# Kernel tuning notes

Measured on AMD Instinct MI355X. Metric: run time of the kernel, lower is better.

## Reference

```python
import jax, jax.numpy as jnp
import numpy as np

EPS = 1e-5  # BatchNorm2d default eps


def _binarize_ste(x):
    """Forward: sign(x). Backward: hardtanh STE (grad 1 where |x|<=1, else 0)."""
    xc = jnp.clip(x, -1.0, 1.0)
    return xc + jax.lax.stop_gradient(jnp.sign(x) - xc)


def setup_inputs() -> dict:
    key = jax.random.key(0)
    k1, k2, k3, k4 = jax.random.split(key, 4)
    x = jax.random.normal(k1, (32, 256, 32, 32), dtype=jnp.float32)
    # BatchNorm affine params (affine=True)
    gamma = 1.0 + 0.1 * jax.random.normal(k2, (256,), dtype=jnp.float32)
    beta = 0.1 * jax.random.normal(k3, (256,), dtype=jnp.float32)
    # Conv weight, OIHW, bias=False
    W = 0.05 * jax.random.normal(k4, (256, 256, 3, 3), dtype=jnp.float32)
    return {"x": x, "gamma": gamma, "beta": beta, "W": W}


def reference(x, gamma, beta, W):
    # BatchNorm2d, training-mode batch statistics over (N, H, W) per channel
    mean = jnp.mean(x, axis=(0, 2, 3), keepdims=True)
    var = jnp.var(x, axis=(0, 2, 3), keepdims=True)
    xn = (x - mean) * jax.lax.rsqrt(var + EPS)
    xn = xn * gamma[None, :, None, None] + beta[None, :, None, None]
    # Conv2d_1w1a: binarize activations and weights (sign fwd / STE bwd), then conv
    a = _binarize_ste(xn)
    wb = _binarize_ste(W)
    out = jax.lax.conv_general_dilated(
        a, wb,
        window_strides=(1, 1),
        padding=((1, 1), (1, 1)),
        dimension_numbers=("NCHW", "OIHW", "NCHW"),
    )
    return out
```

## Files before the change

kernel.cpp:

```cpp
#include <hip/hip_runtime.h>
#include <hip/hip_bf16.h>


#define NIMG 32
#define C    256
#define K    256

typedef int v4i  __attribute__((ext_vector_type(4)));
typedef int v16i __attribute__((ext_vector_type(16)));

#define AHT_IMG 295936
#define AHT_KB  36992
#define AHT_ROW 1088

__global__ __launch_bounds__(256) void k_stats_part(
    const float* __restrict__ x, double2* __restrict__ partials) {
  int grp = blockIdx.x;
  int c = blockIdx.y;
  int tid = threadIdx.x;
  double s = 0.0, sq = 0.0;
  #pragma unroll
  for (int ni = 0; ni < 4; ++ni) {
    int n = grp * 4 + ni;
    const float* p = x + (size_t)n * (C * 1024) + (size_t)c * 1024;
    float4 v = ((const float4*)p)[tid];
    s += (double)v.x + (double)v.y + (double)v.z + (double)v.w;
    sq += (double)v.x * v.x + (double)v.y * v.y
        + (double)v.z * v.z + (double)v.w * v.w;
  }
  for (int o = 32; o > 0; o >>= 1) {
    s += __shfl_down(s, o);
    sq += __shfl_down(sq, o);
  }
  __shared__ double ls[4], lq[4];
  if ((tid & 63) == 0) { ls[tid >> 6] = s; lq[tid >> 6] = sq; }
  __syncthreads();
  if (tid == 0) {
    double2 r;
    r.x = ls[0] + ls[1] + ls[2] + ls[3];
    r.y = lq[0] + lq[1] + lq[2] + lq[3];
    partials[c * 8 + grp] = r;
  }
}


__global__ __launch_bounds__(256) void k_packw_i8_final(
    const float* __restrict__ W, const double2* __restrict__ partials,
    const float* __restrict__ gamma, const float* __restrict__ beta,
    char* __restrict__ wfrag, float* __restrict__ t_out,
    unsigned* __restrict__ flip_out) {
  int bk = blockIdx.x;
  int tid = threadIdx.x;
  if (bk == 256) {
    int c = tid;
    double S = 0.0, Q = 0.0;
    #pragma unroll
    for (int g = 0; g < 8; ++g) {
      double2 p = partials[c * 8 + g];
      S += p.x; Q += p.y;
    }
    const double N = 32768.0;
    double mean = S / N;
    double var = Q / N - mean * mean;
    double rs = 1.0 / sqrt(var + 1e-5);
    double g = (double)gamma[c];
    double b = (double)beta[c];
    float t;
    unsigned flip;
    if (g == 0.0) {
      t = (b > 0.0) ? -3.0e38f : 3.0e38f;
      flip = 0u;
    } else {
      t = (float)(mean - b / (rs * g));
      flip = (g < 0.0) ? 1u : 0u;
    }
    t_out[c] = t;
    flip_out[c] = flip;
    return;
  }
  int k = bk, c = tid;
  const float* src = W + ((size_t)k * 256 + c) * 9;
  char* dst = wfrag + (size_t)(c >> 4) * 4096 + k * 16 + (c & 15);
  #pragma unroll
  for (int t = 0; t < 9; ++t)
    dst[(size_t)t * 65536] = (src[t] > 0.0f) ? (char)1 : (char)-1;
}

__global__ __launch_bounds__(256) void k_packa_i8(
    const float* __restrict__ x, const float* __restrict__ thr,
    const unsigned* __restrict__ flip, char* __restrict__ aHT) {
  __shared__ float lf[32 * 257];
  __shared__ float lthr[256];
  __shared__ unsigned lfl[256];
  int y = blockIdx.x, n = blockIdx.y, tid = threadIdx.x;
  lthr[tid] = thr[tid];
  lfl[tid] = flip[tid];
  #pragma unroll
  for (int it = 0; it < 8; ++it) {
    int c = it * 32 + (tid >> 3), q = tid & 7;
    float4 v = *(const float4*)(x + (size_t)n * 262144 + (size_t)c * 1024
                                + y * 32 + q * 4);
    lf[(q * 4 + 0) * 257 + c] = v.x;
    lf[(q * 4 + 1) * 257 + c] = v.y;
    lf[(q * 4 + 2) * 257 + c] = v.z;
    lf[(q * 4 + 3) * 257 + c] = v.w;
  }
  __syncthreads();
  int xl = tid & 31, cb = tid >> 5;
  unsigned wds[8];
  #pragma unroll
  for (int g = 0; g < 8; ++g) {
    unsigned wv = 0;
    #pragma unroll
    for (int jj = 0; jj < 4; ++jj) {
      int c = cb * 32 + g * 4 + jj;
      float v = lf[xl * 257 + c];
      unsigned bit = ((v > lthr[c]) ? 1u : 0u) ^ lfl[c];
      unsigned byte = bit ? 0x01u : 0xFFu;
      wv |= byte << (8 * jj);
    }
    wds[g] = wv;
  }
  char* dst = aHT + ((size_t)n * 8 + cb) * AHT_KB
            + (size_t)(y + 1) * AHT_ROW + (size_t)(xl + 1) * 32;
  uint4 u0, u1;
  u0.x = wds[0]; u0.y = wds[1]; u0.z = wds[2]; u0.w = wds[3];
  u1.x = wds[4]; u1.y = wds[5]; u1.z = wds[6]; u1.w = wds[7];
  *(uint4*)dst = u0;
  *((uint4*)dst + 1) = u1;

  uint4 z; z.x = 0; z.y = 0; z.z = 0; z.w = 0;
  if (xl < 2) {
    char* hz = aHT + ((size_t)n * 8 + cb) * AHT_KB
             + (size_t)(y + 1) * AHT_ROW + (size_t)(xl * 33) * 32;
    *(uint4*)hz = z;
    *((uint4*)hz + 1) = z;
  }
  if (y == 0 || y == 31) {
    int row = (y == 0) ? 0 : 33;
    for (int idx = tid; idx < 272; idx += 256) {
      int kb = idx / 34, xx = idx % 34;
      char* hz = aHT + ((size_t)n * 8 + kb) * AHT_KB
               + (size_t)row * AHT_ROW + (size_t)xx * 32;
      *(uint4*)hz = z;
      *((uint4*)hz + 1) = z;
    }
  }
}

__global__ __launch_bounds__(256) void k_conv_mfma(
    const char* __restrict__ aHT, const char* __restrict__ wfrag,
    float* __restrict__ out) {
  __shared__ uint4 lb4[2048];
  char* lb = (char*)lb4;
  int tid = threadIdx.x;
  int lane = tid & 63, nh = tid >> 6;
  int bx = blockIdx.x;
  int n = bx >> 4, ys = bx & 15;
  int y0 = ys * 2;
  int xl = lane & 31, hi = lane >> 5;

  const char* abT = aHT + (size_t)n * AHT_IMG + (size_t)(xl + 1) * 32 + hi * 16;
  const char* wsrc0 = wfrag + tid * 16;
  unsigned ldso = (unsigned)(tid * 16);
  unsigned bofs = (unsigned)(hi * 4096 + (nh * 64 + xl) * 16);

  v16i a00 = {0}, a01 = {0}, a10 = {0}, a11 = {0};
  v4i cA00, cA01, cA10, cA11;
  v4i nA00, nA01, nA10, nA11;
  uint4 wt0, wt1, wt2, wt3;

  cA00 = *(const v4i*)(abT + (size_t)(y0 + 0) * AHT_ROW - 32);
  cA01 = *(const v4i*)(abT + (size_t)(y0 + 1) * AHT_ROW - 32);
  cA10 = *(const v4i*)(abT + AHT_KB + (size_t)(y0 + 0) * AHT_ROW - 32);
  cA11 = *(const v4i*)(abT + AHT_KB + (size_t)(y0 + 1) * AHT_ROW - 32);
  wt0 = *(const uint4*)(wsrc0 + 0 * 4096);
  wt1 = *(const uint4*)(wsrc0 + 1 * 4096);
  wt2 = *(const uint4*)(wsrc0 + 2 * 4096);
  wt3 = *(const uint4*)(wsrc0 + 3 * 4096);
  *(uint4*)(lb + 0 * 4096 + ldso) = wt0;
  *(uint4*)(lb + 1 * 4096 + ldso) = wt1;
  *(uint4*)(lb + 2 * 4096 + ldso) = wt2;
  *(uint4*)(lb + 3 * 4096 + ldso) = wt3;
  __syncthreads();

  for (int p = 0; p < 36; ++p) {
    int buf = (p & 1) << 14;
    int nbuf = 16384 - buf;
    if (p < 35) {
      int kk0 = 2 * (p + 1);
      int tt = kk0 >> 3, kb0 = kk0 & 7;
      int dy = tt / 3 - 1, dx = (tt % 3) - 1;
      const char* ab = abT + (size_t)kb0 * AHT_KB
                     + (size_t)(y0 + dy + 1) * AHT_ROW + dx * 32;
      nA00 = *(const v4i*)(ab);
      nA01 = *(const v4i*)(ab + AHT_ROW);
      nA10 = *(const v4i*)(ab + AHT_KB);
      nA11 = *(const v4i*)(ab + AHT_KB + AHT_ROW);
      const char* wsrc = wsrc0 + (size_t)kk0 * 8192;
      wt0 = *(const uint4*)(wsrc + 0 * 4096);
      wt1 = *(const uint4*)(wsrc + 1 * 4096);
      wt2 = *(const uint4*)(wsrc + 2 * 4096);
      wt3 = *(const uint4*)(wsrc + 3 * 4096);
    }
    {
      const char* bp0 = lb + buf + bofs;
      v4i b0 = *(const v4i*)(bp0);
      v4i b1 = *(const v4i*)(bp0 + 512);
      a00 = __builtin_amdgcn_mfma_i32_32x32x32_i8(cA00, b0, a00, 0, 0, 0);
      a01 = __builtin_amdgcn_mfma_i32_32x32x32_i8(cA00, b1, a01, 0, 0, 0);
      a10 = __builtin_amdgcn_mfma_i32_32x32x32_i8(cA01, b0, a10, 0, 0, 0);
      a11 = __builtin_amdgcn_mfma_i32_32x32x32_i8(cA01, b1, a11, 0, 0, 0);
      const char* bp1 = lb + buf + 8192 + bofs;
      v4i b2 = *(const v4i*)(bp1);
      v4i b3 = *(const v4i*)(bp1 + 512);
      a00 = __builtin_amdgcn_mfma_i32_32x32x32_i8(cA10, b2, a00, 0, 0, 0);
      a01 = __builtin_amdgcn_mfma_i32_32x32x32_i8(cA10, b3, a01, 0, 0, 0);
      a10 = __builtin_amdgcn_mfma_i32_32x32x32_i8(cA11, b2, a10, 0, 0, 0);
      a11 = __builtin_amdgcn_mfma_i32_32x32x32_i8(cA11, b3, a11, 0, 0, 0);
    }
    if (p < 35) {
      cA00 = nA00; cA01 = nA01; cA10 = nA10; cA11 = nA11;
      *(uint4*)(lb + nbuf + 0 * 4096 + ldso) = wt0;
      *(uint4*)(lb + nbuf + 1 * 4096 + ldso) = wt1;
      *(uint4*)(lb + nbuf + 2 * 4096 + ldso) = wt2;
      *(uint4*)(lb + nbuf + 3 * 4096 + ldso) = wt3;
      __syncthreads();
    }
  }

  size_t ob0 = (size_t)n * 262144 + (size_t)(nh * 64 + xl) * 1024
             + (size_t)y0 * 32 + 4 * hi;
  #pragma unroll
  for (int r = 0; r < 2; ++r) {
    #pragma unroll
    for (int nb = 0; nb < 2; ++nb) {
      v16i av = (r == 0) ? (nb == 0 ? a00 : a01) : (nb == 0 ? a10 : a11);
      float* obp = out + ob0 + (size_t)nb * 32768 + r * 32;
      #pragma unroll
      for (int q = 0; q < 4; ++q) {
        float4 f;
        f.x = (float)av[q * 4 + 0];
        f.y = (float)av[q * 4 + 1];
        f.z = (float)av[q * 4 + 2];
        f.w = (float)av[q * 4 + 3];
        *(float4*)(obp + 8 * q) = f;
      }
    }
  }
}


__global__ __launch_bounds__(256) void k_packw_corr_final(
    const float* __restrict__ W, const double2* __restrict__ partials,
    const float* __restrict__ gamma, const float* __restrict__ beta,
    unsigned* __restrict__ wp, int* __restrict__ corr,
    unsigned* __restrict__ zp, float* __restrict__ t_out,
    unsigned* __restrict__ flip_out) {
  int bk = blockIdx.x;
  int tid = threadIdx.x;
  if (bk == 256) {
    int c = tid;
    double S = 0.0, Q = 0.0;
    #pragma unroll
    for (int g = 0; g < 8; ++g) {
      double2 p = partials[c * 8 + g];
      S += p.x; Q += p.y;
    }
    const double N = 32768.0;
    double mean = S / N;
    double var = Q / N - mean * mean;
    double rs = 1.0 / sqrt(var + 1e-5);
    double g = (double)gamma[c];
    double b = (double)beta[c];
    float t;
    unsigned flip;
    if (g == 0.0) {
      t = (b > 0.0) ? -3.0e38f : 3.0e38f;
      flip = 0u;
    } else {
      t = (float)(mean - b / (rs * g));
      flip = (g < 0.0) ? 1u : 0u;
    }
    t_out[c] = t;
    flip_out[c] = flip;
    return;
  }
  int k = bk;
  __shared__ unsigned lw[72];
  float w[9];
  const float* src = W + (size_t)k * 2304 + (size_t)tid * 9;
  #pragma unroll
  for (int t = 0; t < 9; ++t) w[t] = src[t];
  int lane = tid & 63, wv = tid >> 6;
  #pragma unroll
  for (int t = 0; t < 9; ++t) {
    unsigned long long m = __ballot(w[t] > 0.0f);
    if (lane == 0) {
      lw[t * 8 + 2 * wv] = (unsigned)m;
      lw[t * 8 + 2 * wv + 1] = (unsigned)(m >> 32);
    }
  }
  __syncthreads();
  if (tid < 72) wp[(size_t)k * 72 + tid] = lw[tid];
  if (tid >= 128 && tid < 144) {
    int cls = tid - 128;
    int sum = 0;
    #pragma unroll
    for (int t = 0; t < 9; ++t) {
      int dy = t / 3 - 1, dx = t % 3 - 1;
      bool inv = (((cls & 1) && dx == -1) || ((cls & 2) && dx == 1) ||
                  ((cls & 4) && dy == -1) || ((cls & 8) && dy == 1));
      if (inv) {
        #pragma unroll
        for (int j = 0; j < 8; ++j) sum += __popc(lw[t * 8 + j]);
      }
    }
    corr[k * 16 + cls] = sum;
  }
  if (bk == 0 && tid >= 192 && tid < 200) zp[tid - 192] = 0u;
}

__global__ __launch_bounds__(256) void k_packa_bits(
    const float* __restrict__ x, const float* __restrict__ t,
    const unsigned* __restrict__ flip, unsigned* __restrict__ ap) {
  int n = blockIdx.y;
  int p0 = blockIdx.x * 64;
  int pix = threadIdx.x & 63;
  int q = threadIdx.x >> 6;
  unsigned w0 = 0, w1 = 0;
  const float* xb = x + (size_t)n * (C * 1024) + p0 + pix;
  #pragma unroll
  for (int i = 0; i < 64; ++i) {
    int c = q * 64 + i;
    float tv = t[c];
    unsigned fl = flip[c];
    float v = xb[(size_t)c * 1024];
    unsigned bit = ((v > tv) ? 1u : 0u) ^ fl;
    if (i < 32) w0 |= bit << i;
    else        w1 |= bit << (i - 32);
  }
  uint2 st; st.x = w0; st.y = w1;
  *(uint2*)(ap + ((size_t)n * 1024 + p0 + pix) * 8 + q * 2) = st;
}

__global__ __launch_bounds__(256) void k_conv_pop(
    const unsigned* __restrict__ ap, const unsigned* __restrict__ wp,
    const int* __restrict__ corr, const unsigned* __restrict__ zp,
    float* __restrict__ out) {
  int n = blockIdx.z;
  int ystrip = blockIdx.y;
  int kc = blockIdx.x;
  int tid = threadIdx.x;
  int lane = tid & 63;
  int wave = tid >> 6;
  int y = ystrip * 8 + wave * 2 + (lane >> 5);
  int xx = lane & 31;
  int cls = (xx == 0 ? 1 : 0) | (xx == 31 ? 2 : 0) |
            (y == 0 ? 4 : 0) | (y == 31 ? 8 : 0);
  uint4 a0[9], a1[9];
  int nv = 0;
  const uint4* zp4 = (const uint4*)zp;
  #pragma unroll
  for (int t = 0; t < 9; ++t) {
    int dy = t / 3 - 1, dx = t % 3 - 1;
    int cy = y + dy, cx = xx + dx;
    bool valid = (cy >= 0) & (cy < 32) & (cx >= 0) & (cx < 32);
    nv += valid ? 1 : 0;
    const uint4* pa = valid
        ? (const uint4*)(ap + (((size_t)n * 32 + cy) * 32 + cx) * 8)
        : zp4;
    a0[t] = pa[0];
    a1[t] = pa[1];
  }
  int bias = nv << 8;
  float* ob = out + (size_t)n * (K * 1024) + (size_t)y * 32 + xx;
  for (int kk = 0; kk < 16; ++kk) {
    int k = kc * 16 + kk;
    const uint4* wq = (const uint4*)(wp + (size_t)k * 72);
    int s0 = 0, s1 = 0, s2 = 0, s3 = 0, s4 = 0, s5 = 0, s6 = 0, s7 = 0;
    #pragma unroll
    for (int t = 0; t < 9; ++t) {
      uint4 wa = wq[t * 2];
      uint4 wb = wq[t * 2 + 1];
      s0 += __popc(a0[t].x ^ wa.x);
      s1 += __popc(a0[t].y ^ wa.y);
      s2 += __popc(a0[t].z ^ wa.z);
      s3 += __popc(a0[t].w ^ wa.w);
      s4 += __popc(a1[t].x ^ wb.x);
      s5 += __popc(a1[t].y ^ wb.y);
      s6 += __popc(a1[t].z ^ wb.z);
      s7 += __popc(a1[t].w ^ wb.w);
    }
    int S = ((s0 + s1) + (s2 + s3)) + ((s4 + s5) + (s6 + s7));
    int tot = corr[(k << 4) + cls] - S;
    ob[(size_t)k * 1024] = (float)(bias + 2 * tot);
  }
}


extern "C" void kernel_launch(void* const* d_in, const int* in_sizes, int n_in,
                              void* d_out, int out_size, void* d_ws, size_t ws_size,
                              hipStream_t stream) {
  const float* x = (const float*)d_in[0];
  const float* gamma = (const float*)d_in[1];
  const float* beta = (const float*)d_in[2];
  const float* W = (const float*)d_in[3];
  float* out = (float*)d_out;
  char* ws = (char*)d_ws;

  const size_t NEED = 655360 + (size_t)NIMG * AHT_IMG;
  if (ws_size >= NEED) {
    float* t = (float*)ws;
    unsigned* flip = (unsigned*)(ws + 1024);
    double2* partials = (double2*)(ws + 4096);
    char* wfrag = ws + 36864;
    char* aHT = ws + 655360;

    k_stats_part<<<dim3(8, 256), 256, 0, stream>>>(x, partials);
    k_packw_i8_final<<<257, 256, 0, stream>>>(W, partials, gamma, beta,
                                              wfrag, t, flip);
    k_packa_i8<<<dim3(32, 32), 256, 0, stream>>>(x, t, flip, aHT);
    k_conv_mfma<<<512, 256, 0, stream>>>(aHT, wfrag, out);
  } else {
    float* t = (float*)ws;
    unsigned* flip = (unsigned*)(ws + 1024);
    unsigned* wp = (unsigned*)(ws + 4096);
    unsigned* zp = (unsigned*)(ws + 77824);
    int* corr = (int*)(ws + 78336);
    double2* partials = (double2*)(ws + 98304);
    unsigned* ap = (unsigned*)(ws + 131072);

    k_stats_part<<<dim3(8, 256), 256, 0, stream>>>(x, partials);
    k_packw_corr_final<<<257, 256, 0, stream>>>(W, partials, gamma, beta,
                                                wp, corr, zp, t, flip);
    k_packa_bits<<<dim3(16, 32), 256, 0, stream>>>(x, t, flip, ap);
    k_conv_pop<<<dim3(16, 4, 32), 256, 0, stream>>>(ap, wp, corr, zp, out);
  }
}
```

Baseline: 54.33 us.

## Share LDS weight tiles across two row-pairs with 512-thread conv blocks

The MFMA conv kernel now runs 512-thread blocks, 256 of them, and each block covers four output rows instead of two. Two groups of four waves share each LDS weight stage, so every thread loads half as many weight vectors per stage and total weight traffic from global memory is halved. The cost is fewer, larger blocks (256 for 256 CUs), a larger barrier scope and possibly lower occupancy.

```diff
diff --git a/kernel.cpp b/kernel.cpp
--- a/kernel.cpp
+++ b/kernel.cpp
@@ -148,60 +148,58 @@
   }
 }
 
-__global__ __launch_bounds__(256) void k_conv_mfma(
+__global__ __launch_bounds__(512) void k_conv_mfma(
     const char* __restrict__ aHT, const char* __restrict__ wfrag,
     float* __restrict__ out) {
   __shared__ uint4 lb4[2048];
   char* lb = (char*)lb4;
   int tid = threadIdx.x;
-  int lane = tid & 63, nh = tid >> 6;
+  int lane = tid & 63, w = tid >> 6;
   int bx = blockIdx.x;
-  int n = bx >> 4, ys = bx & 15;
-  int y0 = ys * 2;
+  int n = bx >> 3, ys = bx & 7;
+  int mb = w >> 2, nh = w & 3;
+  int yw = ys * 4 + mb * 2;
   int xl = lane & 31, hi = lane >> 5;
 
   const char* abT = aHT + (size_t)n * AHT_IMG + (size_t)(xl + 1) * 32 + hi * 16;
-  const char* wsrc0 = wfrag + tid * 16;
-  unsigned ldso = (unsigned)(tid * 16);
+  const char* wsrcA = wfrag + tid * 16;
+  unsigned ldsoA = (unsigned)(tid * 16);
   unsigned bofs = (unsigned)(hi * 4096 + (nh * 64 + xl) * 16);
 
   v16i a00 = {0}, a01 = {0}, a10 = {0}, a11 = {0};
   v4i cA00, cA01, cA10, cA11;
   v4i nA00, nA01, nA10, nA11;
-  uint4 wt0, wt1, wt2, wt3;
-
-  cA00 = *(const v4i*)(abT + (size_t)(y0 + 0) * AHT_ROW - 32);
-  cA01 = *(const v4i*)(abT + (size_t)(y0 + 1) * AHT_ROW - 32);
-  cA10 = *(const v4i*)(abT + AHT_KB + (size_t)(y0 + 0) * AHT_ROW - 32);
-  cA11 = *(const v4i*)(abT + AHT_KB + (size_t)(y0 + 1) * AHT_ROW - 32);
-  wt0 = *(const uint4*)(wsrc0 + 0 * 4096);
-  wt1 = *(const uint4*)(wsrc0 + 1 * 4096);
-  wt2 = *(const uint4*)(wsrc0 + 2 * 4096);
-  wt3 = *(const uint4*)(wsrc0 + 3 * 4096);
-  *(uint4*)(lb + 0 * 4096 + ldso) = wt0;
-  *(uint4*)(lb + 1 * 4096 + ldso) = wt1;
-  *(uint4*)(lb + 2 * 4096 + ldso) = wt2;
-  *(uint4*)(lb + 3 * 4096 + ldso) = wt3;
+  uint4 wt0, wt1;
+
+  {
+    const char* ab = abT + (size_t)yw * AHT_ROW - 32;
+    cA00 = *(const v4i*)(ab);
+    cA01 = *(const v4i*)(ab + AHT_ROW);
+    cA10 = *(const v4i*)(ab + AHT_KB);
+    cA11 = *(const v4i*)(ab + AHT_KB + AHT_ROW);
+    uint4 s0 = *(const uint4*)(wsrcA);
+    uint4 s1 = *(const uint4*)(wsrcA + 8192);
+    *(uint4*)(lb + ldsoA) = s0;
+    *(uint4*)(lb + 8192 + ldsoA) = s1;
+  }
   __syncthreads();
 
   for (int p = 0; p < 36; ++p) {
     int buf = (p & 1) << 14;
-    int nbuf = 16384 - buf;
     if (p < 35) {
-      int kk0 = 2 * (p + 1);
-      int tt = kk0 >> 3, kb0 = kk0 & 7;
-      int dy = tt / 3 - 1, dx = (tt % 3) - 1;
+      int pp = p + 1;
+      int tt = pp >> 2;
+      int kb0 = (pp & 3) * 2;
+      int dy = tt / 3 - 1, dx = tt % 3 - 1;
       const char* ab = abT + (size_t)kb0 * AHT_KB
-                     + (size_t)(y0 + dy + 1) * AHT_ROW + dx * 32;
+                     + (size_t)(yw + dy + 1) * AHT_ROW + dx * 32;
       nA00 = *(const v4i*)(ab);
       nA01 = *(const v4i*)(ab + AHT_ROW);
       nA10 = *(const v4i*)(ab + AHT_KB);
       nA11 = *(const v4i*)(ab + AHT_KB + AHT_ROW);
-      const char* wsrc = wsrc0 + (size_t)kk0 * 8192;
-      wt0 = *(const uint4*)(wsrc + 0 * 4096);
-      wt1 = *(const uint4*)(wsrc + 1 * 4096);
-      wt2 = *(const uint4*)(wsrc + 2 * 4096);
-      wt3 = *(const uint4*)(wsrc + 3 * 4096);
+      const char* wsrc = wsrcA + (size_t)pp * 16384;
+      wt0 = *(const uint4*)(wsrc);
+      wt1 = *(const uint4*)(wsrc + 8192);
     }
     {
       const char* bp0 = lb + buf + bofs;
@@ -221,16 +219,15 @@
     }
     if (p < 35) {
       cA00 = nA00; cA01 = nA01; cA10 = nA10; cA11 = nA11;
-      *(uint4*)(lb + nbuf + 0 * 4096 + ldso) = wt0;
-      *(uint4*)(lb + nbuf + 1 * 4096 + ldso) = wt1;
-      *(uint4*)(lb + nbuf + 2 * 4096 + ldso) = wt2;
-      *(uint4*)(lb + nbuf + 3 * 4096 + ldso) = wt3;
+      int nbuf = 16384 - buf;
+      *(uint4*)(lb + nbuf + ldsoA) = wt0;
+      *(uint4*)(lb + nbuf + 8192 + ldsoA) = wt1;
       __syncthreads();
     }
   }
 
   size_t ob0 = (size_t)n * 262144 + (size_t)(nh * 64 + xl) * 1024
-             + (size_t)y0 * 32 + 4 * hi;
+             + (size_t)yw * 32 + 4 * hi;
   #pragma unroll
   for (int r = 0; r < 2; ++r) {
     #pragma unroll
@@ -421,7 +418,7 @@
     k_packw_i8_final<<<257, 256, 0, stream>>>(W, partials, gamma, beta,
                                               wfrag, t, flip);
     k_packa_i8<<<dim3(32, 32), 256, 0, stream>>>(x, t, flip, aHT);
-    k_conv_mfma<<<512, 256, 0, stream>>>(aHT, wfrag, out);
+    k_conv_mfma<<<256, 512, 0, stream>>>(aHT, wfrag, out);
   } else {
     float* t = (float*)ws;
     unsigned* flip = (unsigned*)(ws + 1024);
```

After: 57.35 us. 5.6% more time.
